# Kernel optimization log

Measured on AMD Instinct MI355X. Metric: run time of the kernel, lower is better.

Reference implementation:

```python
import jax, jax.numpy as jnp
import numpy as np

B, T, C, H = 2, 2048, 2048, 16
HD = C // H      # 128 head dim
P = C // 8       # 256 octonion component width
NEG_INF = jnp.finfo(jnp.float32).min

# Cayley octonion multiplication table: e_i * e_j = OCT_SIGN[i,j] * e_{OCT_IDX[i,j]}
OCT_SIGN = np.array([
    [1, 1, 1, 1, 1, 1, 1, 1],
    [1,-1, 1,-1, 1,-1,-1, 1],
    [1,-1,-1, 1, 1, 1,-1,-1],
    [1, 1,-1,-1, 1,-1, 1,-1],
    [1,-1,-1,-1,-1, 1, 1, 1],
    [1, 1,-1, 1,-1,-1,-1, 1],
    [1, 1, 1,-1,-1, 1,-1,-1],
    [1,-1, 1, 1,-1,-1, 1,-1]], dtype=np.float32)
OCT_IDX = np.array([
    [0,1,2,3,4,5,6,7],
    [1,0,3,2,5,4,7,6],
    [2,3,0,1,6,7,4,5],
    [3,2,1,0,7,6,5,4],
    [4,5,6,7,0,1,2,3],
    [5,4,7,6,1,0,3,2],
    [6,7,4,5,2,3,0,1],
    [7,6,5,4,3,2,1,0]], dtype=np.int32)
_comb = np.zeros((8, 8, 8), np.float32)
for _i in range(8):
    for _j in range(8):
        _comb[OCT_IDX[_i, _j], _i, _j] = OCT_SIGN[_i, _j]
COMB = jnp.asarray(_comb)  # (k, i, j): out_k += sign * (W_i @ x_j)


def ternary(W):
    # BitNet-style ternary quantization with straight-through estimator
    s = jnp.mean(jnp.abs(W)) + 1e-8
    q = jnp.round(jnp.clip(W / s, -1.0, 1.0)) * s
    return W + jax.lax.stop_gradient(q - W)


def oct_linear(x, W):
    # x: (B,T,C), W: (8,P,P) -> (B,T,C)
    parts = jnp.stack(jnp.split(x, 8, axis=-1), axis=0)  # (8,B,T,P)
    Wq = ternary(W)
    prod = jnp.einsum('jbtp,ipq->ijbtq', parts, Wq)       # (8,8,B,T,P)
    out = jnp.einsum('kij,ijbtq->kbtq', COMB, prod)       # (8,B,T,P)
    return jnp.transpose(out, (1, 2, 0, 3)).reshape(x.shape[0], x.shape[1], C)


def rope(x, cos, sin):
    # x: (B,T,H,HD); cos/sin: (T, HD//2). Interleaved complex pairs as in view_as_complex.
    xr = x[..., 0::2]
    xi = x[..., 1::2]
    c = cos[None, :x.shape[1], None, :]
    s = sin[None, :x.shape[1], None, :]
    out = jnp.stack([xr * c - xi * s, xr * s + xi * c], axis=-1)
    return out.reshape(x.shape)


def setup_inputs() -> dict:
    key = jax.random.key(0)
    ks = jax.random.split(key, 5)
    x = jax.random.normal(ks[0], (B, T, C), dtype=jnp.float32)
    wq = jax.random.normal(ks[1], (8, P, P), dtype=jnp.float32) * 0.02
    wk = jax.random.normal(ks[2], (8, P, P), dtype=jnp.float32) * 0.02
    wv = jax.random.normal(ks[3], (8, P, P), dtype=jnp.float32) * 0.02
    wo = jax.random.normal(ks[4], (8, P, P), dtype=jnp.float32) * 0.02
    inv = 1.0 / (10000.0 ** (np.arange(0, HD, 2, dtype=np.float32) / HD))
    ang = np.outer(np.arange(T, dtype=np.float32), inv)
    freqs_cos = jnp.asarray(np.cos(ang), dtype=jnp.float32)
    freqs_sin = jnp.asarray(np.sin(ang), dtype=jnp.float32)
    return {"x": x, "wq": wq, "wk": wk, "wv": wv, "wo": wo,
            "freqs_cos": freqs_cos, "freqs_sin": freqs_sin}


def reference(x, wq, wk, wv, wo, freqs_cos, freqs_sin):
    b, t, _ = x.shape
    q = oct_linear(x, wq).reshape(b, t, H, HD)
    k = oct_linear(x, wk).reshape(b, t, H, HD)
    v = oct_linear(x, wv).reshape(b, t, H, HD)
    q = rope(q, freqs_cos, freqs_sin)
    k = rope(k, freqs_cos, freqs_sin)
    q = jnp.transpose(q, (0, 2, 1, 3))  # (B,H,T,HD)
    k = jnp.transpose(k, (0, 2, 1, 3))
    v = jnp.transpose(v, (0, 2, 1, 3))
    scores = jnp.einsum('bhtd,bhsd->bhts', q, k) / jnp.sqrt(jnp.float32(HD))
    mask = jnp.tril(jnp.ones((t, t), dtype=bool))
    scores = jnp.where(mask[None, None], scores, NEG_INF)
    attn = jax.nn.softmax(scores, axis=-1)
    y = jnp.einsum('bhts,bhsd->bhtd', attn, v)
    y = jnp.transpose(y, (0, 2, 1, 3)).reshape(b, t, C)
    return oct_linear(y, wo)
```

## Files before the change

### kernel.cpp

```cpp
#include <hip/hip_runtime.h>


typedef __attribute__((ext_vector_type(8))) short short8;
typedef __attribute__((ext_vector_type(4))) float f32x4;
typedef unsigned short u16;
typedef unsigned int u32;

__device__ __forceinline__ float bf2f(u16 u) {
    u32 x = ((u32)u) << 16;
    return __builtin_bit_cast(float, x);
}
__device__ __forceinline__ u16 f2bf(float f) {
    u32 x = __builtin_bit_cast(u32, f);
    x += 0x7fffu + ((x >> 16) & 1u);
    return (u16)(x >> 16);
}
__device__ __forceinline__ u16 f2bf_trunc(float f) {
    return (u16)(__builtin_bit_cast(u32, f) >> 16);
}
__device__ __forceinline__ u32 pack2(u16 a, u16 b) { return (u32)a | ((u32)b << 16); }

__device__ __forceinline__ void async16(const void* g, void* l) {
    __builtin_amdgcn_global_load_lds((const __attribute__((address_space(1))) u32*)g,
                                     (__attribute__((address_space(3))) u32*)l, 16, 0, 0);
}

__device__ const int d_OCT_IDX[8][8] = {
    {0,1,2,3,4,5,6,7},{1,0,3,2,5,4,7,6},{2,3,0,1,6,7,4,5},{3,2,1,0,7,6,5,4},
    {4,5,6,7,0,1,2,3},{5,4,7,6,1,0,3,2},{6,7,4,5,2,3,0,1},{7,6,5,4,3,2,1,0}};
__device__ const float d_OCT_SIGN[8][8] = {
    { 1, 1, 1, 1, 1, 1, 1, 1},{ 1,-1, 1,-1, 1,-1,-1, 1},{ 1,-1,-1, 1, 1, 1,-1,-1},
    { 1, 1,-1,-1, 1,-1, 1,-1},{ 1,-1,-1,-1,-1, 1, 1, 1},{ 1, 1,-1, 1,-1,-1,-1, 1},
    { 1, 1, 1,-1,-1, 1,-1,-1},{ 1,-1, 1, 1,-1,-1, 1,-1}};

__global__ __launch_bounds__(256) void reduce1_kernel(
    const float* __restrict__ w0, const float* __restrict__ w1,
    const float* __restrict__ w2, const float* __restrict__ w3,
    float* __restrict__ partials) {
    int bid = blockIdx.x, wsel = bid >> 6, part = bid & 63;
    const float* W = wsel == 0 ? w0 : wsel == 1 ? w1 : wsel == 2 ? w2 : w3;
    int base = part * 8192 + threadIdx.x;
    float acc = 0.f;
#pragma unroll
    for (int k = 0; k < 32; k++) acc += fabsf(W[base + k * 256]);
#pragma unroll
    for (int off = 1; off < 64; off <<= 1) acc += __shfl_xor(acc, off, 64);
    __shared__ float r4[4];
    if ((threadIdx.x & 63) == 0) r4[threadIdx.x >> 6] = acc;
    __syncthreads();
    if (threadIdx.x == 0) partials[bid] = r4[0] + r4[1] + r4[2] + r4[3];
}
__global__ __launch_bounds__(256) void reduce2_kernel(const float* __restrict__ partials,
                                                      float* __restrict__ s_vals) {
    int w = threadIdx.x >> 6, lane = threadIdx.x & 63;
    float v = partials[w * 64 + lane];
#pragma unroll
    for (int off = 1; off < 64; off <<= 1) v += __shfl_xor(v, off, 64);
    if (lane == 0) s_vals[w] = v / 524288.0f + 1e-8f;
}

__global__ __launch_bounds__(256) void cast_bf16_kernel(const float* __restrict__ X, u16* __restrict__ Xb) {
    int gid = blockIdx.x * 256 + threadIdx.x;
    const float4* X4 = (const float4*)X;
    float4 a = X4[gid * 2], b = X4[gid * 2 + 1];
    uint4 o;
    o.x = pack2(f2bf(a.x), f2bf(a.y));
    o.y = pack2(f2bf(a.z), f2bf(a.w));
    o.z = pack2(f2bf(b.x), f2bf(b.y));
    o.w = pack2(f2bf(b.z), f2bf(b.w));
    *(uint4*)&Xb[gid * 8] = o;
}

__global__ __launch_bounds__(256) void build_weff_kernel(
    const float* __restrict__ W, const float* __restrict__ sptr, u16* __restrict__ WT) {
    __shared__ float Tt[64 * 68];
    int tid = threadIdx.x;
    int combo = blockIdx.x >> 4, sub = blockIdx.x & 15;
    int j = combo >> 3, kblk = combo & 7;
    int i = 0;
#pragma unroll
    for (int ii = 0; ii < 8; ii++)
        if (d_OCT_IDX[ii][j] == kblk) i = ii;
    float sign = d_OCT_SIGN[i][j];
    int p0 = (sub >> 2) * 64, q0 = (sub & 3) * 64;
    float inv_s = 1.0f / (*sptr);
#pragma unroll
    for (int pass = 0; pass < 4; pass++) {
        int p = p0 + pass * 16 + (tid >> 4);
        int q = q0 + (tid & 15) * 4;
        float4 wv = *(const float4*)&W[i * 65536 + p * 256 + q];
        float* Tp = &Tt[(pass * 16 + (tid >> 4)) * 68 + (tid & 15) * 4];
        Tp[0] = sign * rintf(fminf(1.f, fmaxf(-1.f, wv.x * inv_s)));
        Tp[1] = sign * rintf(fminf(1.f, fmaxf(-1.f, wv.y * inv_s)));
        Tp[2] = sign * rintf(fminf(1.f, fmaxf(-1.f, wv.z * inv_s)));
        Tp[3] = sign * rintf(fminf(1.f, fmaxf(-1.f, wv.w * inv_s)));
    }
    __syncthreads();
#pragma unroll
    for (int pass = 0; pass < 2; pass++) {
        int qq = pass * 32 + (tid >> 3);
        int pl = (tid & 7) * 8;
        u16 r[8];
#pragma unroll
        for (int l = 0; l < 8; l++) r[l] = f2bf_trunc(Tt[(pl + l) * 68 + qq]);
        uint4 o;
        o.x = pack2(r[0], r[1]); o.y = pack2(r[2], r[3]);
        o.z = pack2(r[4], r[5]); o.w = pack2(r[6], r[7]);
        *(uint4*)&WT[(size_t)(kblk * 256 + q0 + qq) * 2048 + j * 256 + p0 + pl] = o;
    }
}

template <int MODE>
__global__ __launch_bounds__(256) void gemm_kernel(
    const u16* __restrict__ A, const u16* __restrict__ Bt,
    const float* __restrict__ sptr, void* __restrict__ Cout) {
    __shared__ __align__(16) u16 As[2][128 * 64];
    __shared__ __align__(16) u16 Bs[2][128 * 64];
    const int K = 2048;
    const int NIT = K / 64;
    int tid = threadIdx.x, lane = tid & 63, wid = tid >> 6;
    int quad = lane >> 4, l16 = lane & 15;
    int wm = (wid >> 1) * 64, wn = (wid & 1) * 64;
    int m0 = blockIdx.y * 128, n0 = blockIdx.x * 128;
    f32x4 acc[4][4];
#pragma unroll
    for (int a = 0; a < 4; a++)
#pragma unroll
        for (int b = 0; b < 4; b++) acc[a][b] = (f32x4){0.f, 0.f, 0.f, 0.f};
    int sr = lane >> 3, sb = lane & 7;
    const u16* Ag = A + (size_t)(m0 + wid * 32 + sr) * K + ((sb ^ sr) * 8);
    const u16* Bg = Bt + (size_t)(n0 + wid * 32 + sr) * K + ((sb ^ sr) * 8);
#pragma unroll
    for (int cc = 0; cc < 4; cc++) {
        async16(Ag + (size_t)cc * 8 * K, &As[0][(wid * 32 + cc * 8) * 64]);
        async16(Bg + (size_t)cc * 8 * K, &Bs[0][(wid * 32 + cc * 8) * 64]);
    }
    for (int g = 0; g < NIT; g++) {
        int c = g & 1;
        __syncthreads();
        if (g + 1 < NIT) {
            int k1 = (g + 1) * 64;
#pragma unroll
            for (int cc = 0; cc < 4; cc++) {
                async16(Ag + k1 + (size_t)cc * 8 * K, &As[1 - c][(wid * 32 + cc * 8) * 64]);
                async16(Bg + k1 + (size_t)cc * 8 * K, &Bs[1 - c][(wid * 32 + cc * 8) * 64]);
            }
        }
#pragma unroll
        for (int kc = 0; kc < 2; kc++) {
            short8 af[4], bfv[4];
#pragma unroll
            for (int mt = 0; mt < 4; mt++)
                af[mt] = *(const short8*)&As[c][(wm + mt * 16 + l16) * 64 + (((kc << 2) | quad) ^ (l16 & 7)) * 8];
#pragma unroll
            for (int nt = 0; nt < 4; nt++)
                bfv[nt] = *(const short8*)&Bs[c][(wn + nt * 16 + l16) * 64 + (((kc << 2) | quad) ^ (l16 & 7)) * 8];
#pragma unroll
            for (int mt = 0; mt < 4; mt++)
#pragma unroll
                for (int nt = 0; nt < 4; nt++)
                    acc[mt][nt] = __builtin_amdgcn_mfma_f32_16x16x32_bf16(af[mt], bfv[nt], acc[mt][nt], 0, 0, 0);
        }
    }
    float s = *sptr;
#pragma unroll
    for (int mt = 0; mt < 4; mt++)
#pragma unroll
        for (int nt = 0; nt < 4; nt++) {
            int mg = m0 + wm + mt * 16 + quad * 4;
            int ng = n0 + wn + nt * 16 + l16;
            if (MODE == 0) {
#pragma unroll
                for (int r = 0; r < 4; r++)
                    ((u16*)Cout)[(size_t)(mg + r) * 2048 + ng] = f2bf(acc[mt][nt][r] * s);
            } else if (MODE == 1) {
#pragma unroll
                for (int r = 0; r < 4; r++)
                    ((float*)Cout)[(size_t)(mg + r) * 2048 + ng] = acc[mt][nt][r] * s;
            } else {
                ushort4 o4;
                o4.x = f2bf(acc[mt][nt][0] * s);
                o4.y = f2bf(acc[mt][nt][1] * s);
                o4.z = f2bf(acc[mt][nt][2] * s);
                o4.w = f2bf(acc[mt][nt][3] * s);
                *(ushort4*)&((u16*)Cout)[((size_t)((mg >> 11) * 16 + (ng >> 7)) * 128 + (ng & 127)) * 2048 + (mg & 2047)] = o4;
            }
        }
}

__device__ __forceinline__ u32 rope_rot(u32 u, float c, float s) {
    float xr = bf2f((u16)(u & 0xffff));
    float xi = bf2f((u16)(u >> 16));
    return pack2(f2bf(xr * c - xi * s), f2bf(xr * s + xi * c));
}
__global__ __launch_bounds__(256) void rope_kernel(
    u16* __restrict__ Xb, const float* __restrict__ fc, const float* __restrict__ fs, float scale) {
    int gid = blockIdx.x * 256 + threadIdx.x;
    int e0 = gid * 4;
    int t = (e0 >> 10) & 2047;
    int m = e0 & 63;
    uint4 u = ((const uint4*)Xb)[gid];
    float4 c4 = *(const float4*)&fc[t * 64 + m];
    float4 s4 = *(const float4*)&fs[t * 64 + m];
    uint4 o;
    o.x = rope_rot(u.x, c4.x * scale, s4.x * scale);
    o.y = rope_rot(u.y, c4.y * scale, s4.y * scale);
    o.z = rope_rot(u.z, c4.z * scale, s4.z * scale);
    o.w = rope_rot(u.w, c4.w * scale, s4.w * scale);
    ((uint4*)Xb)[gid] = o;
}

__global__ __launch_bounds__(512, 2) void flash_kernel(
    const u16* __restrict__ Q, const u16* __restrict__ Kg,
    const u16* __restrict__ VTg, u16* __restrict__ Y) {
    __shared__ __align__(16) u16 Ks[2][64 * 128];
    __shared__ __align__(16) u16 Vs[2][128 * 64];
    __shared__ __align__(16) u16 Ps[8 * 16 * 64];
    const int NIT = 34;
    int tid = threadIdx.x, lane = tid & 63, wid = tid >> 6;
    int quad = lane >> 4, l16 = lane & 15;
    int bh = blockIdx.x, b = bh >> 4, h = bh & 15;
    int qt = blockIdx.y;
    int nitA = 2 * qt + 2;
    const u16* Qb = Q + (size_t)b * 2048 * 2048 + h * 128;
    const u16* Kb = Kg + (size_t)b * 2048 * 2048 + h * 128;
    const u16* Vb = VTg + (size_t)bh * 128 * 2048;
    int q0 = qt * 128, nit = nitA;
    int ksr = lane >> 4, ksb = lane & 15;
    int vsr = lane >> 3, vsb = lane & 7;
#pragma unroll
    for (int cc = 0; cc < 2; cc++) {
        int ch = wid * 2 + cc;
        int kr = ch * 4 + ksr;
        async16(&Kb[(size_t)kr * 2048 + (ksb ^ (kr & 15)) * 8], &Ks[0][ch * 512]);
        int vd = ch * 8 + vsr;
        async16(&Vb[(size_t)vd * 2048 + (vsb ^ (vd & 7)) * 8], &Vs[0][ch * 512]);
    }
    short8 qf[4];
#pragma unroll
    for (int kt = 0; kt < 4; kt++)
        qf[kt] = *(const short8*)&Qb[(size_t)(q0 + wid * 16 + l16) * 2048 + kt * 32 + quad * 8];
    f32x4 o[8];
#pragma unroll
    for (int nt = 0; nt < 8; nt++) o[nt] = (f32x4){0.f, 0.f, 0.f, 0.f};
    float m_[4] = {-1e30f, -1e30f, -1e30f, -1e30f};
    float l_[4] = {0.f, 0.f, 0.f, 0.f};
    int il = 0;
    for (int g = 0; g < NIT; g++) {
        int c = g & 1;
        __syncthreads();
        if (g + 1 < NIT) {
            int gn = g + 1;
            int s0n = (gn < nitA ? gn : gn - nitA) * 64;
#pragma unroll
            for (int cc = 0; cc < 2; cc++) {
                int ch = wid * 2 + cc;
                int kr = ch * 4 + ksr;
                async16(&Kb[(size_t)(s0n + kr) * 2048 + (ksb ^ (kr & 15)) * 8], &Ks[1 - c][ch * 512]);
                int vd = ch * 8 + vsr;
                async16(&Vb[(size_t)vd * 2048 + s0n + (vsb ^ (vd & 7)) * 8], &Vs[1 - c][ch * 512]);
            }
        }
        int s0 = il * 64;
        f32x4 sc[4];
        __builtin_amdgcn_s_setprio(1);
#pragma unroll
        for (int ct = 0; ct < 4; ct++) {
            f32x4 a = (f32x4){0.f, 0.f, 0.f, 0.f};
#pragma unroll
            for (int kt = 0; kt < 4; kt++) {
                short8 bfv = *(const short8*)&Ks[c][(ct * 16 + l16) * 128 + ((kt * 4 + quad) ^ l16) * 8];
                a = __builtin_amdgcn_mfma_f32_16x16x32_bf16(qf[kt], bfv, a, 0, 0, 0);
            }
            sc[ct] = a;
        }
        __builtin_amdgcn_s_setprio(0);
        if (il >= nit - 2) {
#pragma unroll
            for (int ct = 0; ct < 4; ct++) {
                int colg = s0 + ct * 16 + l16;
#pragma unroll
                for (int r = 0; r < 4; r++) {
                    int rowg = q0 + wid * 16 + quad * 4 + r;
                    if (colg > rowg) sc[ct][r] = -1e30f;
                }
            }
        }
        float alpha[4];
#pragma unroll
        for (int r = 0; r < 4; r++) {
            float mx = fmaxf(fmaxf(sc[0][r], sc[1][r]), fmaxf(sc[2][r], sc[3][r]));
#pragma unroll
            for (int off = 1; off < 16; off <<= 1) mx = fmaxf(mx, __shfl_xor(mx, off, 64));
            float mn = fmaxf(m_[r], mx);
            float al = exp2f(m_[r] - mn);
            float rs = 0.f;
#pragma unroll
            for (int ct = 0; ct < 4; ct++) {
                float p = exp2f(sc[ct][r] - mn);
                sc[ct][r] = p;
                rs += p;
            }
#pragma unroll
            for (int off = 1; off < 16; off <<= 1) rs += __shfl_xor(rs, off, 64);
            m_[r] = mn;
            l_[r] = l_[r] * al + rs;
            alpha[r] = al;
        }
        u16* Pw = &Ps[wid * 1024];
#pragma unroll
        for (int ct = 0; ct < 4; ct++)
#pragma unroll
            for (int r = 0; r < 4; r++) {
                int lr = quad * 4 + r;
                int key = ct * 16 + l16;
                Pw[lr * 64 + ((key >> 3) ^ (lr & 7)) * 8 + (key & 7)] = f2bf_trunc(sc[ct][r]);
            }
#pragma unroll
        for (int nt = 0; nt < 8; nt++)
#pragma unroll
            for (int r = 0; r < 4; r++) o[nt][r] *= alpha[r];
        __builtin_amdgcn_s_setprio(1);
#pragma unroll
        for (int kt2 = 0; kt2 < 2; kt2++) {
            short8 pa = *(const short8*)&Pw[l16 * 64 + ((kt2 * 4 + quad) ^ (l16 & 7)) * 8];
#pragma unroll
            for (int nt = 0; nt < 8; nt++) {
                short8 vb = *(const short8*)&Vs[c][(nt * 16 + l16) * 64 + ((kt2 * 4 + quad) ^ (l16 & 7)) * 8];
                o[nt] = __builtin_amdgcn_mfma_f32_16x16x32_bf16(pa, vb, o[nt], 0, 0, 0);
            }
        }
        __builtin_amdgcn_s_setprio(0);
        il++;
        if (il == nit && g + 1 < NIT) {
            float iv[4];
#pragma unroll
            for (int r = 0; r < 4; r++) iv[r] = 1.f / l_[r];
#pragma unroll
            for (int nt = 0; nt < 8; nt++)
#pragma unroll
                for (int r = 0; r < 4; r++) {
                    int t_ = q0 + wid * 16 + quad * 4 + r;
                    Y[((size_t)(b * 2048 + t_)) * 2048 + h * 128 + nt * 16 + l16] = f2bf(o[nt][r] * iv[r]);
                }
            q0 = (15 - qt) * 128;
            nit = NIT - nitA;
            il = 0;
#pragma unroll
            for (int kt = 0; kt < 4; kt++)
                qf[kt] = *(const short8*)&Qb[(size_t)(q0 + wid * 16 + l16) * 2048 + kt * 32 + quad * 8];
#pragma unroll
            for (int nt = 0; nt < 8; nt++) o[nt] = (f32x4){0.f, 0.f, 0.f, 0.f};
#pragma unroll
            for (int r = 0; r < 4; r++) { m_[r] = -1e30f; l_[r] = 0.f; }
        }
    }
    float iv[4];
#pragma unroll
    for (int r = 0; r < 4; r++) iv[r] = 1.f / l_[r];
#pragma unroll
    for (int nt = 0; nt < 8; nt++)
#pragma unroll
        for (int r = 0; r < 4; r++) {
            int t_ = q0 + wid * 16 + quad * 4 + r;
            Y[((size_t)(b * 2048 + t_)) * 2048 + h * 128 + nt * 16 + l16] = f2bf(o[nt][r] * iv[r]);
        }
}

extern "C" void kernel_launch(void* const* d_in, const int* in_sizes, int n_in,
                              void* d_out, int out_size, void* d_ws, size_t ws_size,
                              hipStream_t stream) {
    const float* x  = (const float*)d_in[0];
    const float* wq = (const float*)d_in[1];
    const float* wk = (const float*)d_in[2];
    const float* wv = (const float*)d_in[3];
    const float* wo = (const float*)d_in[4];
    const float* fc = (const float*)d_in[5];
    const float* fs = (const float*)d_in[6];
    float* out = (float*)d_out;

    char* ws = (char*)d_ws;
    float* s_vals   = (float*)ws;
    float* partials = (float*)(ws + 1024);
    u16* WT  = (u16*)(ws + 8192);
    u16* xb  = (u16*)(ws + 8192 + 8388608);
    u16* Qb  = xb + 8388608;
    u16* Kb  = Qb + 8388608;
    u16* VTb = Kb + 8388608;

    const float QSCALE = 0.08838834764831845f * 1.4426950408889634f;

    reduce1_kernel<<<256, 256, 0, stream>>>(wq, wk, wv, wo, partials);
    reduce2_kernel<<<1, 256, 0, stream>>>(partials, s_vals);
    cast_bf16_kernel<<<4096, 256, 0, stream>>>(x, xb);

    build_weff_kernel<<<1024, 256, 0, stream>>>(wq, s_vals + 0, WT);
    gemm_kernel<0><<<dim3(16, 32), 256, 0, stream>>>(xb, WT, s_vals + 0, Qb);
    rope_kernel<<<4096, 256, 0, stream>>>(Qb, fc, fs, QSCALE);

    build_weff_kernel<<<1024, 256, 0, stream>>>(wk, s_vals + 1, WT);
    gemm_kernel<0><<<dim3(16, 32), 256, 0, stream>>>(xb, WT, s_vals + 1, Kb);
    rope_kernel<<<4096, 256, 0, stream>>>(Kb, fc, fs, 1.0f);

    build_weff_kernel<<<1024, 256, 0, stream>>>(wv, s_vals + 2, WT);
    gemm_kernel<2><<<dim3(16, 32), 256, 0, stream>>>(xb, WT, s_vals + 2, VTb);

    flash_kernel<<<dim3(32, 8), 512, 0, stream>>>(Qb, Kb, VTb, Qb );

    build_weff_kernel<<<1024, 256, 0, stream>>>(wo, s_vals + 3, WT);
    gemm_kernel<1><<<dim3(16, 32), 256, 0, stream>>>(Qb, WT, s_vals + 3, (void*)out);
}
```

Before: 399.4 us.

## Split paired causal q-tiles into separate blocks and register-stage V

```diff
diff --git a/kernel.cpp b/kernel.cpp
--- a/kernel.cpp
+++ b/kernel.cpp
@@ -210,32 +210,34 @@
     ((uint4*)Xb)[gid] = o;
 }
 
-__global__ __launch_bounds__(512, 2) void flash_kernel(
+__global__ __launch_bounds__(512, 4) void flash_kernel(
     const u16* __restrict__ Q, const u16* __restrict__ Kg,
     const u16* __restrict__ VTg, u16* __restrict__ Y) {
     __shared__ __align__(16) u16 Ks[2][64 * 128];
-    __shared__ __align__(16) u16 Vs[2][128 * 64];
+    __shared__ __align__(16) u16 Vs[128 * 64];
     __shared__ __align__(16) u16 Ps[8 * 16 * 64];
-    const int NIT = 34;
     int tid = threadIdx.x, lane = tid & 63, wid = tid >> 6;
     int quad = lane >> 4, l16 = lane & 15;
     int bh = blockIdx.x, b = bh >> 4, h = bh & 15;
-    int qt = blockIdx.y;
-    int nitA = 2 * qt + 2;
+    int y = blockIdx.y;
+    int qt = (y < 8) ? (15 - 2 * y) : (2 * (y - 8));
+    int nit = 2 * (qt + 1);
+    int q0 = qt * 128;
     const u16* Qb = Q + (size_t)b * 2048 * 2048 + h * 128;
     const u16* Kb = Kg + (size_t)b * 2048 * 2048 + h * 128;
     const u16* Vb = VTg + (size_t)bh * 128 * 2048;
-    int q0 = qt * 128, nit = nitA;
     int ksr = lane >> 4, ksb = lane & 15;
-    int vsr = lane >> 3, vsb = lane & 7;
+    int vd = tid >> 2, vs0 = (tid & 3) * 2;
 #pragma unroll
     for (int cc = 0; cc < 2; cc++) {
         int ch = wid * 2 + cc;
         int kr = ch * 4 + ksr;
         async16(&Kb[(size_t)kr * 2048 + (ksb ^ (kr & 15)) * 8], &Ks[0][ch * 512]);
-        int vd = ch * 8 + vsr;
-        async16(&Vb[(size_t)vd * 2048 + (vsb ^ (vd & 7)) * 8], &Vs[0][ch * 512]);
-    }
+    }
+    uint4 vreg[2];
+#pragma unroll
+    for (int j = 0; j < 2; j++)
+        vreg[j] = *(const uint4*)&Vb[(size_t)vd * 2048 + (vs0 + j) * 8];
     short8 qf[4];
 #pragma unroll
     for (int kt = 0; kt < 4; kt++)
@@ -245,25 +247,26 @@
     for (int nt = 0; nt < 8; nt++) o[nt] = (f32x4){0.f, 0.f, 0.f, 0.f};
     float m_[4] = {-1e30f, -1e30f, -1e30f, -1e30f};
     float l_[4] = {0.f, 0.f, 0.f, 0.f};
-    int il = 0;
-    for (int g = 0; g < NIT; g++) {
+    for (int g = 0; g < nit; g++) {
         int c = g & 1;
         __syncthreads();
-        if (g + 1 < NIT) {
-            int gn = g + 1;
-            int s0n = (gn < nitA ? gn : gn - nitA) * 64;
+#pragma unroll
+        for (int j = 0; j < 2; j++)
+            *(uint4*)&Vs[vd * 64 + ((vs0 + j) ^ (vd & 7)) * 8] = vreg[j];
+        if (g + 1 < nit) {
+            int s0n = (g + 1) * 64;
 #pragma unroll
             for (int cc = 0; cc < 2; cc++) {
                 int ch = wid * 2 + cc;
                 int kr = ch * 4 + ksr;
                 async16(&Kb[(size_t)(s0n + kr) * 2048 + (ksb ^ (kr & 15)) * 8], &Ks[1 - c][ch * 512]);
-                int vd = ch * 8 + vsr;
-                async16(&Vb[(size_t)vd * 2048 + s0n + (vsb ^ (vd & 7)) * 8], &Vs[1 - c][ch * 512]);
-            }
-        }
-        int s0 = il * 64;
+            }
+#pragma unroll
+            for (int j = 0; j < 2; j++)
+                vreg[j] = *(const uint4*)&Vb[(size_t)vd * 2048 + s0n + (vs0 + j) * 8];
+        }
+        int s0 = g * 64;
         f32x4 sc[4];
-        __builtin_amdgcn_s_setprio(1);
 #pragma unroll
         for (int ct = 0; ct < 4; ct++) {
             f32x4 a = (f32x4){0.f, 0.f, 0.f, 0.f};
@@ -274,8 +277,7 @@
             }
             sc[ct] = a;
         }
-        __builtin_amdgcn_s_setprio(0);
-        if (il >= nit - 2) {
+        if (g >= nit - 2) {
 #pragma unroll
             for (int ct = 0; ct < 4; ct++) {
                 int colg = s0 + ct * 16 + l16;
@@ -320,39 +322,17 @@
         for (int nt = 0; nt < 8; nt++)
 #pragma unroll
             for (int r = 0; r < 4; r++) o[nt][r] *= alpha[r];
-        __builtin_amdgcn_s_setprio(1);
+        asm volatile("s_waitcnt lgkmcnt(0)" ::: "memory");
+        __builtin_amdgcn_sched_barrier(0);
+        __builtin_amdgcn_s_barrier();
 #pragma unroll
         for (int kt2 = 0; kt2 < 2; kt2++) {
             short8 pa = *(const short8*)&Pw[l16 * 64 + ((kt2 * 4 + quad) ^ (l16 & 7)) * 8];
 #pragma unroll
             for (int nt = 0; nt < 8; nt++) {
-                short8 vb = *(const short8*)&Vs[c][(nt * 16 + l16) * 64 + ((kt2 * 4 + quad) ^ (l16 & 7)) * 8];
+                short8 vb = *(const short8*)&Vs[(nt * 16 + l16) * 64 + ((kt2 * 4 + quad) ^ (l16 & 7)) * 8];
                 o[nt] = __builtin_amdgcn_mfma_f32_16x16x32_bf16(pa, vb, o[nt], 0, 0, 0);
             }
-        }
-        __builtin_amdgcn_s_setprio(0);
-        il++;
-        if (il == nit && g + 1 < NIT) {
-            float iv[4];
-#pragma unroll
-            for (int r = 0; r < 4; r++) iv[r] = 1.f / l_[r];
-#pragma unroll
-            for (int nt = 0; nt < 8; nt++)
-#pragma unroll
-                for (int r = 0; r < 4; r++) {
-                    int t_ = q0 + wid * 16 + quad * 4 + r;
-                    Y[((size_t)(b * 2048 + t_)) * 2048 + h * 128 + nt * 16 + l16] = f2bf(o[nt][r] * iv[r]);
-                }
-            q0 = (15 - qt) * 128;
-            nit = NIT - nitA;
-            il = 0;
-#pragma unroll
-            for (int kt = 0; kt < 4; kt++)
-                qf[kt] = *(const short8*)&Qb[(size_t)(q0 + wid * 16 + l16) * 2048 + kt * 32 + quad * 8];
-#pragma unroll
-            for (int nt = 0; nt < 8; nt++) o[nt] = (f32x4){0.f, 0.f, 0.f, 0.f};
-#pragma unroll
-            for (int r = 0; r < 4; r++) { m_[r] = -1e30f; l_[r] = 0.f; }
         }
     }
     float iv[4];
@@ -405,7 +385,7 @@
     build_weff_kernel<<<1024, 256, 0, stream>>>(wv, s_vals + 2, WT);
     gemm_kernel<2><<<dim3(16, 32), 256, 0, stream>>>(xb, WT, s_vals + 2, VTb);
 
-    flash_kernel<<<dim3(32, 8), 512, 0, stream>>>(Qb, Kb, VTb, Qb );
+    flash_kernel<<<dim3(32, 16), 512, 0, stream>>>(Qb, Kb, VTb, Qb );
 
     build_weff_kernel<<<1024, 256, 0, stream>>>(wo, s_vals + 3, WT);
     gemm_kernel<1><<<dim3(16, 32), 256, 0, stream>>>(Qb, WT, s_vals + 3, (void*)out);
```

New measurement: 442.8 us. +10.9%, slower.

## Enlarge GEMM tile to 256x128 with 512 threads and triple-buffered async loads

Applied to the files above, without the earlier changes.

```diff
diff --git a/kernel.cpp b/kernel.cpp
--- a/kernel.cpp
+++ b/kernel.cpp
@@ -111,17 +111,17 @@
 }
 
 template <int MODE>
-__global__ __launch_bounds__(256) void gemm_kernel(
+__global__ __launch_bounds__(512, 2) void gemm_kernel(
     const u16* __restrict__ A, const u16* __restrict__ Bt,
     const float* __restrict__ sptr, void* __restrict__ Cout) {
-    __shared__ __align__(16) u16 As[2][128 * 64];
-    __shared__ __align__(16) u16 Bs[2][128 * 64];
+    __shared__ __align__(16) u16 As[3][256 * 64];
+    __shared__ __align__(16) u16 Bs[3][128 * 64];
     const int K = 2048;
     const int NIT = K / 64;
     int tid = threadIdx.x, lane = tid & 63, wid = tid >> 6;
     int quad = lane >> 4, l16 = lane & 15;
     int wm = (wid >> 1) * 64, wn = (wid & 1) * 64;
-    int m0 = blockIdx.y * 128, n0 = blockIdx.x * 128;
+    int m0 = blockIdx.y * 256, n0 = blockIdx.x * 128;
     f32x4 acc[4][4];
 #pragma unroll
     for (int a = 0; a < 4; a++)
@@ -129,38 +129,45 @@
         for (int b = 0; b < 4; b++) acc[a][b] = (f32x4){0.f, 0.f, 0.f, 0.f};
     int sr = lane >> 3, sb = lane & 7;
     const u16* Ag = A + (size_t)(m0 + wid * 32 + sr) * K + ((sb ^ sr) * 8);
-    const u16* Bg = Bt + (size_t)(n0 + wid * 32 + sr) * K + ((sb ^ sr) * 8);
-#pragma unroll
-    for (int cc = 0; cc < 4; cc++) {
-        async16(Ag + (size_t)cc * 8 * K, &As[0][(wid * 32 + cc * 8) * 64]);
-        async16(Bg + (size_t)cc * 8 * K, &Bs[0][(wid * 32 + cc * 8) * 64]);
-    }
-    for (int g = 0; g < NIT; g++) {
-        int c = g & 1;
-        __syncthreads();
-        if (g + 1 < NIT) {
-            int k1 = (g + 1) * 64;
-#pragma unroll
-            for (int cc = 0; cc < 4; cc++) {
-                async16(Ag + k1 + (size_t)cc * 8 * K, &As[1 - c][(wid * 32 + cc * 8) * 64]);
-                async16(Bg + k1 + (size_t)cc * 8 * K, &Bs[1 - c][(wid * 32 + cc * 8) * 64]);
-            }
+    const u16* Bg = Bt + (size_t)(n0 + wid * 16 + sr) * K + ((sb ^ sr) * 8);
+    auto issue = [&](int t, int bi) {
+        int k = t * 64;
+#pragma unroll
+        for (int cc = 0; cc < 4; cc++)
+            async16(Ag + k + (size_t)cc * 8 * K, &As[bi][(wid * 32 + cc * 8) * 64]);
+#pragma unroll
+        for (int cc = 0; cc < 2; cc++)
+            async16(Bg + k + (size_t)cc * 8 * K, &Bs[bi][(wid * 16 + cc * 8) * 64]);
+    };
+    issue(0, 0);
+    issue(1, 1);
+    int bi = 0;
+    for (int g = 0; g < NIT; ++g) {
+        if (g + 1 < NIT) asm volatile("s_waitcnt vmcnt(6)" ::: "memory");
+        else             asm volatile("s_waitcnt vmcnt(0)" ::: "memory");
+        __builtin_amdgcn_s_barrier();
+        asm volatile("" ::: "memory");
+        __builtin_amdgcn_sched_barrier(0);
+        if (g + 2 < NIT) {
+            int bn = bi + 2; if (bn >= 3) bn -= 3;
+            issue(g + 2, bn);
         }
 #pragma unroll
         for (int kc = 0; kc < 2; kc++) {
             short8 af[4], bfv[4];
 #pragma unroll
             for (int mt = 0; mt < 4; mt++)
-                af[mt] = *(const short8*)&As[c][(wm + mt * 16 + l16) * 64 + (((kc << 2) | quad) ^ (l16 & 7)) * 8];
+                af[mt] = *(const short8*)&As[bi][(wm + mt * 16 + l16) * 64 + (((kc << 2) | quad) ^ (l16 & 7)) * 8];
 #pragma unroll
             for (int nt = 0; nt < 4; nt++)
-                bfv[nt] = *(const short8*)&Bs[c][(wn + nt * 16 + l16) * 64 + (((kc << 2) | quad) ^ (l16 & 7)) * 8];
+                bfv[nt] = *(const short8*)&Bs[bi][(wn + nt * 16 + l16) * 64 + (((kc << 2) | quad) ^ (l16 & 7)) * 8];
 #pragma unroll
             for (int mt = 0; mt < 4; mt++)
 #pragma unroll
                 for (int nt = 0; nt < 4; nt++)
                     acc[mt][nt] = __builtin_amdgcn_mfma_f32_16x16x32_bf16(af[mt], bfv[nt], acc[mt][nt], 0, 0, 0);
         }
+        bi++; if (bi == 3) bi = 0;
     }
     float s = *sptr;
 #pragma unroll
@@ -263,7 +270,6 @@
         }
         int s0 = il * 64;
         f32x4 sc[4];
-        __builtin_amdgcn_s_setprio(1);
 #pragma unroll
         for (int ct = 0; ct < 4; ct++) {
             f32x4 a = (f32x4){0.f, 0.f, 0.f, 0.f};
@@ -274,7 +280,6 @@
             }
             sc[ct] = a;
         }
-        __builtin_amdgcn_s_setprio(0);
         if (il >= nit - 2) {
 #pragma unroll
             for (int ct = 0; ct < 4; ct++) {
@@ -320,7 +325,6 @@
         for (int nt = 0; nt < 8; nt++)
 #pragma unroll
             for (int r = 0; r < 4; r++) o[nt][r] *= alpha[r];
-        __builtin_amdgcn_s_setprio(1);
 #pragma unroll
         for (int kt2 = 0; kt2 < 2; kt2++) {
             short8 pa = *(const short8*)&Pw[l16 * 64 + ((kt2 * 4 + quad) ^ (l16 & 7)) * 8];
@@ -330,7 +334,6 @@
                 o[nt] = __builtin_amdgcn_mfma_f32_16x16x32_bf16(pa, vb, o[nt], 0, 0, 0);
             }
         }
-        __builtin_amdgcn_s_setprio(0);
         il++;
         if (il == nit && g + 1 < NIT) {
             float iv[4];
@@ -395,18 +398,18 @@
     cast_bf16_kernel<<<4096, 256, 0, stream>>>(x, xb);
 
     build_weff_kernel<<<1024, 256, 0, stream>>>(wq, s_vals + 0, WT);
-    gemm_kernel<0><<<dim3(16, 32), 256, 0, stream>>>(xb, WT, s_vals + 0, Qb);
+    gemm_kernel<0><<<dim3(16, 16), 512, 0, stream>>>(xb, WT, s_vals + 0, Qb);
     rope_kernel<<<4096, 256, 0, stream>>>(Qb, fc, fs, QSCALE);
 
     build_weff_kernel<<<1024, 256, 0, stream>>>(wk, s_vals + 1, WT);
-    gemm_kernel<0><<<dim3(16, 32), 256, 0, stream>>>(xb, WT, s_vals + 1, Kb);
+    gemm_kernel<0><<<dim3(16, 16), 512, 0, stream>>>(xb, WT, s_vals + 1, Kb);
     rope_kernel<<<4096, 256, 0, stream>>>(Kb, fc, fs, 1.0f);
 
     build_weff_kernel<<<1024, 256, 0, stream>>>(wv, s_vals + 2, WT);
-    gemm_kernel<2><<<dim3(16, 32), 256, 0, stream>>>(xb, WT, s_vals + 2, VTb);
+    gemm_kernel<2><<<dim3(16, 16), 512, 0, stream>>>(xb, WT, s_vals + 2, VTb);
 
     flash_kernel<<<dim3(32, 8), 512, 0, stream>>>(Qb, Kb, VTb, Qb );
 
     build_weff_kernel<<<1024, 256, 0, stream>>>(wo, s_vals + 3, WT);
-    gemm_kernel<1><<<dim3(16, 32), 256, 0, stream>>>(Qb, WT, s_vals + 3, (void*)out);
-}
+    gemm_kernel<1><<<dim3(16, 16), 512, 0, stream>>>(Qb, WT, s_vals + 3, (void*)out);
+}
```

Result: slower. 451.0 us (+12.9%).

## Single-buffer V via registers, lazy softmax rescale, raise flash occupancy

Applied to the files above, without the earlier changes.

```diff
diff --git a/kernel.cpp b/kernel.cpp
--- a/kernel.cpp
+++ b/kernel.cpp
@@ -210,11 +210,11 @@
     ((uint4*)Xb)[gid] = o;
 }
 
-__global__ __launch_bounds__(512, 2) void flash_kernel(
+__global__ __launch_bounds__(512, 4) void flash_kernel(
     const u16* __restrict__ Q, const u16* __restrict__ Kg,
     const u16* __restrict__ VTg, u16* __restrict__ Y) {
     __shared__ __align__(16) u16 Ks[2][64 * 128];
-    __shared__ __align__(16) u16 Vs[2][128 * 64];
+    __shared__ __align__(16) u16 Vs[128 * 64];
     __shared__ __align__(16) u16 Ps[8 * 16 * 64];
     const int NIT = 34;
     int tid = threadIdx.x, lane = tid & 63, wid = tid >> 6;
@@ -227,15 +227,16 @@
     const u16* Vb = VTg + (size_t)bh * 128 * 2048;
     int q0 = qt * 128, nit = nitA;
     int ksr = lane >> 4, ksb = lane & 15;
-    int vsr = lane >> 3, vsb = lane & 7;
+    int vd0 = wid * 16 + (lane >> 3), vkb = lane & 7;
 #pragma unroll
     for (int cc = 0; cc < 2; cc++) {
         int ch = wid * 2 + cc;
         int kr = ch * 4 + ksr;
         async16(&Kb[(size_t)kr * 2048 + (ksb ^ (kr & 15)) * 8], &Ks[0][ch * 512]);
-        int vd = ch * 8 + vsr;
-        async16(&Vb[(size_t)vd * 2048 + (vsb ^ (vd & 7)) * 8], &Vs[0][ch * 512]);
-    }
+    }
+    uint4 vreg[2];
+    vreg[0] = *(const uint4*)&Vb[(size_t)vd0 * 2048 + vkb * 8];
+    vreg[1] = *(const uint4*)&Vb[(size_t)(vd0 + 8) * 2048 + vkb * 8];
     short8 qf[4];
 #pragma unroll
     for (int kt = 0; kt < 4; kt++)
@@ -249,6 +250,8 @@
     for (int g = 0; g < NIT; g++) {
         int c = g & 1;
         __syncthreads();
+        *(uint4*)&Vs[vd0 * 64 + (vkb ^ (vd0 & 7)) * 8] = vreg[0];
+        *(uint4*)&Vs[(vd0 + 8) * 64 + (vkb ^ ((vd0 + 8) & 7)) * 8] = vreg[1];
         if (g + 1 < NIT) {
             int gn = g + 1;
             int s0n = (gn < nitA ? gn : gn - nitA) * 64;
@@ -257,13 +260,12 @@
                 int ch = wid * 2 + cc;
                 int kr = ch * 4 + ksr;
                 async16(&Kb[(size_t)(s0n + kr) * 2048 + (ksb ^ (kr & 15)) * 8], &Ks[1 - c][ch * 512]);
-                int vd = ch * 8 + vsr;
-                async16(&Vb[(size_t)vd * 2048 + s0n + (vsb ^ (vd & 7)) * 8], &Vs[1 - c][ch * 512]);
-            }
+            }
+            vreg[0] = *(const uint4*)&Vb[(size_t)vd0 * 2048 + s0n + vkb * 8];
+            vreg[1] = *(const uint4*)&Vb[(size_t)(vd0 + 8) * 2048 + s0n + vkb * 8];
         }
         int s0 = il * 64;
         f32x4 sc[4];
-        __builtin_amdgcn_s_setprio(1);
 #pragma unroll
         for (int ct = 0; ct < 4; ct++) {
             f32x4 a = (f32x4){0.f, 0.f, 0.f, 0.f};
@@ -274,7 +276,6 @@
             }
             sc[ct] = a;
         }
-        __builtin_amdgcn_s_setprio(0);
         if (il >= nit - 2) {
 #pragma unroll
             for (int ct = 0; ct < 4; ct++) {
@@ -286,26 +287,42 @@
                 }
             }
         }
-        float alpha[4];
+        float mx[4];
 #pragma unroll
         for (int r = 0; r < 4; r++) {
-            float mx = fmaxf(fmaxf(sc[0][r], sc[1][r]), fmaxf(sc[2][r], sc[3][r]));
-#pragma unroll
-            for (int off = 1; off < 16; off <<= 1) mx = fmaxf(mx, __shfl_xor(mx, off, 64));
-            float mn = fmaxf(m_[r], mx);
-            float al = exp2f(m_[r] - mn);
+            float m2 = fmaxf(fmaxf(sc[0][r], sc[1][r]), fmaxf(sc[2][r], sc[3][r]));
+#pragma unroll
+            for (int off = 1; off < 16; off <<= 1) m2 = fmaxf(m2, __shfl_xor(m2, off, 64));
+            mx[r] = m2;
+        }
+        bool need = (mx[0] > m_[0] + 8.f) || (mx[1] > m_[1] + 8.f) ||
+                    (mx[2] > m_[2] + 8.f) || (mx[3] > m_[3] + 8.f);
+        if (__any(need)) {
+            float alpha[4];
+#pragma unroll
+            for (int r = 0; r < 4; r++) {
+                float mn = fmaxf(m_[r], mx[r]);
+                alpha[r] = exp2f(m_[r] - mn);
+                m_[r] = mn;
+                l_[r] *= alpha[r];
+            }
+#pragma unroll
+            for (int nt = 0; nt < 8; nt++)
+#pragma unroll
+                for (int r = 0; r < 4; r++) o[nt][r] *= alpha[r];
+        }
+#pragma unroll
+        for (int r = 0; r < 4; r++) {
             float rs = 0.f;
 #pragma unroll
             for (int ct = 0; ct < 4; ct++) {
-                float p = exp2f(sc[ct][r] - mn);
+                float p = exp2f(sc[ct][r] - m_[r]);
                 sc[ct][r] = p;
                 rs += p;
             }
 #pragma unroll
             for (int off = 1; off < 16; off <<= 1) rs += __shfl_xor(rs, off, 64);
-            m_[r] = mn;
-            l_[r] = l_[r] * al + rs;
-            alpha[r] = al;
+            l_[r] += rs;
         }
         u16* Pw = &Ps[wid * 1024];
 #pragma unroll
@@ -316,21 +333,18 @@
                 int key = ct * 16 + l16;
                 Pw[lr * 64 + ((key >> 3) ^ (lr & 7)) * 8 + (key & 7)] = f2bf_trunc(sc[ct][r]);
             }
-#pragma unroll
-        for (int nt = 0; nt < 8; nt++)
-#pragma unroll
-            for (int r = 0; r < 4; r++) o[nt][r] *= alpha[r];
-        __builtin_amdgcn_s_setprio(1);
+        asm volatile("s_waitcnt lgkmcnt(0)" ::: "memory");
+        __builtin_amdgcn_sched_barrier(0);
+        __builtin_amdgcn_s_barrier();
 #pragma unroll
         for (int kt2 = 0; kt2 < 2; kt2++) {
             short8 pa = *(const short8*)&Pw[l16 * 64 + ((kt2 * 4 + quad) ^ (l16 & 7)) * 8];
 #pragma unroll
             for (int nt = 0; nt < 8; nt++) {
-                short8 vb = *(const short8*)&Vs[c][(nt * 16 + l16) * 64 + ((kt2 * 4 + quad) ^ (l16 & 7)) * 8];
+                short8 vb = *(const short8*)&Vs[(nt * 16 + l16) * 64 + ((kt2 * 4 + quad) ^ (l16 & 7)) * 8];
                 o[nt] = __builtin_amdgcn_mfma_f32_16x16x32_bf16(pa, vb, o[nt], 0, 0, 0);
             }
         }
-        __builtin_amdgcn_s_setprio(0);
         il++;
         if (il == nit && g + 1 < NIT) {
             float iv[4];
```

Result: slower. 437.9 us (+9.6%).
